# Optimization experiments

Measured on AMD Instinct MI355X. Metric: run time of the kernel, lower is better.

The kernel has to match this reference:

```python
import jax, jax.numpy as jnp
import numpy as np

D_EMBED = 1024
N_HEAD = 16
MAX_SEQ = 512
D_K = D_EMBED // N_HEAD


def setup_inputs() -> dict:
    key = jax.random.key(0)
    ks = jax.random.split(key, 10)
    B, S, D = 16, MAX_SEQ, D_EMBED
    std = 1.0 / np.sqrt(D)
    x = jax.random.normal(ks[0], (B, S, D), dtype=jnp.float32)
    Wq = jax.random.normal(ks[1], (D, D), dtype=jnp.float32) * std
    bq = jnp.zeros((D,), dtype=jnp.float32)
    Wk = jax.random.normal(ks[2], (D, D), dtype=jnp.float32) * std
    bk = jnp.zeros((D,), dtype=jnp.float32)
    Wv = jax.random.normal(ks[3], (D, D), dtype=jnp.float32) * std
    bv = jnp.zeros((D,), dtype=jnp.float32)
    Wo = jax.random.normal(ks[4], (D, D), dtype=jnp.float32) * std
    bo = jnp.zeros((D,), dtype=jnp.float32)
    rel_table = jax.random.normal(ks[5], (2 * MAX_SEQ - 1, N_HEAD), dtype=jnp.float32) * 0.02
    return {"x": x, "Wq": Wq, "bq": bq, "Wk": Wk, "bk": bk,
            "Wv": Wv, "bv": bv, "Wo": Wo, "bo": bo, "rel_table": rel_table}


def reference(x, Wq, bq, Wk, bk, Wv, bv, Wo, bo, rel_table):
    B, S, D = x.shape
    H, dk = N_HEAD, D_K
    scale = 1.0 / np.sqrt(dk)
    # QKV projections -> (B, H, S, dk)
    q = (x @ Wq.T + bq).reshape(B, S, H, dk).transpose(0, 2, 1, 3)
    k = (x @ Wk.T + bk).reshape(B, S, H, dk).transpose(0, 2, 1, 3)
    v = (x @ Wv.T + bv).reshape(B, S, H, dk).transpose(0, 2, 1, 3)
    # raw scores (B, H, S, S)
    scores = jnp.einsum('bhsd,bhtd->bhst', q * scale, k)
    # relative position bias: index[i,j] = i + (S-1-j), table (2S-1, H)
    i = jnp.arange(S)
    idx = i[:, None] + (S - 1 - i)[None, :]          # (S, S)
    bias = rel_table[idx]                             # (S, S, H)
    scores = scores + bias.transpose(2, 0, 1)[None]   # (1, H, S, S)
    probs = jax.nn.softmax(scores, axis=-1)
    attn = jnp.einsum('bhst,bhtd->bhsd', probs, v)
    attn = attn.transpose(0, 2, 1, 3).reshape(B, S, D)
    return attn @ Wo.T + bo
```

## Files before the change

kernel.cpp:

```cpp
#include <hip/hip_runtime.h>
#include <cstdint>
#include <cstddef>

typedef unsigned short u16;
typedef __attribute__((ext_vector_type(8))) short bf16x8;
typedef __attribute__((ext_vector_type(4))) float f32x4;

__device__ __forceinline__ u16 f2bf(float f) {
  unsigned u = __builtin_bit_cast(unsigned, f);
  return (u16)((u + 0x7FFFu + ((u >> 16) & 1u)) >> 16);
}

__device__ __forceinline__ void gload_lds16(const void* g, void* l) {
  __builtin_amdgcn_global_load_lds(
      (const __attribute__((address_space(1))) void*)g,
      (__attribute__((address_space(3))) void*)l,
      16, 0, 0);
}

__global__ void cast_all_kernel(const float* __restrict__ x,
                                const float* __restrict__ wq, const float* __restrict__ wk,
                                const float* __restrict__ wv, const float* __restrict__ wo,
                                u16* __restrict__ ox,
                                u16* __restrict__ oq, u16* __restrict__ ok,
                                u16* __restrict__ ov, u16* __restrict__ oo) {
  const int which = blockIdx.y;
  const float* in = which == 0 ? x  : which == 1 ? wq : which == 2 ? wk
                                    : which == 3 ? wv : wo;
  u16* out        = which == 0 ? ox : which == 1 ? oq : which == 2 ? ok
                                    : which == 3 ? ov : oo;
  const int n4 = which == 0 ? 8192 * 1024 / 4 : 262144;
  int i = blockIdx.x * blockDim.x + threadIdx.x;
  int stride = gridDim.x * blockDim.x;
  for (int idx = i; idx < n4; idx += stride) {
    float4 f = ((const float4*)in)[idx];
    ushort4 o = make_ushort4(f2bf(f.x), f2bf(f.y), f2bf(f.z), f2bf(f.w));
    ((ushort4*)out)[idx] = o;
  }
}


#define STAGE_A8(BUF, H, T)                                                    \
  { const u16* s_ = Asrc + (size_t)(H) * 131072 + (T) * 64;                    \
    u16* d_ = &lds[(BUF) * 32768 + (H) * 8192 + wid * 512];                    \
    gload_lds16(s_, d_);                                                       \
    gload_lds16(s_ + 65536, d_ + 4096); }

#define STAGE_B8(BUF, H, T)                                                    \
  { const u16* s_ = Wsrc + (size_t)(H) * 131072 + (T) * 64;                    \
    u16* d_ = &lds[(BUF) * 32768 + 16384 + (H) * 8192 + wid * 512];            \
    gload_lds16(s_, d_);                                                       \
    gload_lds16(s_ + 65536, d_ + 4096); }

#define LOAD_A8(BUF, MH)                                                       \
  _Pragma("unroll") for (int j_ = 0; j_ < 4; ++j_) {                           \
    const int r_ = ((MH) * 4 + j_) * 16 + lc;                                  \
    const int o_ = (BUF) * 32768 + abase + r_ * 64;                            \
    a[j_][0] = *(const bf16x8*)&lds[o_ + ((g ^ (r_ & 7)) * 8)];                \
    a[j_][1] = *(const bf16x8*)&lds[o_ + (((4 + g) ^ (r_ & 7)) * 8)];          \
  }

#define LOAD_B8(BUF, NH, BREG)                                                 \
  _Pragma("unroll") for (int j_ = 0; j_ < 2; ++j_) {                           \
    const int r_ = brlo + ((NH) * 2 + j_) * 16 + lc;                           \
    const int o_ = (BUF) * 32768 + bbase + r_ * 64;                            \
    BREG[j_][0] = *(const bf16x8*)&lds[o_ + ((g ^ (r_ & 7)) * 8)];             \
    BREG[j_][1] = *(const bf16x8*)&lds[o_ + (((4 + g) ^ (r_ & 7)) * 8)];       \
  }

#define MMAQ8(MH, NH, BREG)                                                    \
  __builtin_amdgcn_s_setprio(1);                                               \
  _Pragma("unroll") for (int j_ = 0; j_ < 4; ++j_)                             \
    _Pragma("unroll") for (int n_ = 0; n_ < 2; ++n_) {                         \
      acc[(MH) * 4 + j_][(NH) * 2 + n_] =                                      \
          __builtin_amdgcn_mfma_f32_16x16x32_bf16(                             \
              a[j_][0], BREG[n_][0], acc[(MH) * 4 + j_][(NH) * 2 + n_], 0, 0, 0); \
      acc[(MH) * 4 + j_][(NH) * 2 + n_] =                                      \
          __builtin_amdgcn_mfma_f32_16x16x32_bf16(                             \
              a[j_][1], BREG[n_][1], acc[(MH) * 4 + j_][(NH) * 2 + n_], 0, 0, 0); \
    }                                                                          \
  __builtin_amdgcn_s_setprio(0);

#define BAR1a                                                                  \
  __builtin_amdgcn_s_barrier();                                                \
  asm volatile("s_waitcnt lgkmcnt(0)" ::: "memory");                           \
  __builtin_amdgcn_sched_barrier(0);

#define BAR2a __builtin_amdgcn_s_barrier();

#define VMW(N) asm volatile("s_waitcnt vmcnt(" #N ")" ::: "memory");

__global__ __launch_bounds__(512, 2)
void gemm_qkv8(const u16* __restrict__ A, const u16* __restrict__ W,
               const float* __restrict__ bq, const float* __restrict__ bk,
               const float* __restrict__ bvv,
               u16* __restrict__ qout, u16* __restrict__ kout, u16* __restrict__ vt) {
  __shared__ u16 lds[65536];
  const int tid  = threadIdx.x;
  const int lane = tid & 63;
  const int wid  = tid >> 6;
  const int wr   = wid >> 2;
  const int wc   = wid & 3;
  const int lc   = lane & 15;
  const int g    = lane >> 4;

  const int orig = blockIdx.x;
  const int swz  = (orig & 7) * 48 + (orig >> 3);
  const int m0 = (swz / 12) * 256;
  const int n0 = (swz % 12) * 256;

  const int srow  = tid >> 3;
  const int scol8 = ((tid & 7) ^ (srow & 7)) * 8;
  const u16* Asrc = A + (size_t)(m0 + srow) * 1024 + scol8;
  const u16* Wsrc = W + (size_t)(n0 + srow) * 1024 + scol8;

  const int abase = wr * 8192;
  const int bbase = 16384 + (wc >> 1) * 8192;
  const int brlo  = (wc & 1) * 64;

  f32x4 acc[8][4] = {};
  bf16x8 a[4][2], bA[2][2], bB[2][2];

  STAGE_B8(0, 0, 0) STAGE_B8(0, 1, 0) STAGE_A8(0, 0, 0) STAGE_A8(0, 1, 0)
  STAGE_B8(1, 0, 1) STAGE_B8(1, 1, 1)
  VMW(4)
  __builtin_amdgcn_s_barrier();

  for (int i = 0; i < 7; ++i) {
    const int tb  = 2 * i + 1;
    const int ta2 = 2 * i + 2;
    const int tb2 = 2 * i + 3;
    LOAD_A8(0, 0) LOAD_B8(0, 0, bA) STAGE_A8(1, 0, tb) BAR1a MMAQ8(0, 0, bA) BAR2a
    LOAD_B8(0, 1, bB) STAGE_A8(1, 1, tb) BAR1a MMAQ8(0, 1, bB) BAR2a
    LOAD_A8(0, 1) STAGE_B8(0, 0, ta2) BAR1a MMAQ8(1, 0, bA) BAR2a
    STAGE_B8(0, 1, ta2) BAR1a MMAQ8(1, 1, bB) VMW(4) BAR2a
    LOAD_A8(1, 0) LOAD_B8(1, 0, bA) STAGE_A8(0, 0, ta2) BAR1a MMAQ8(0, 0, bA) BAR2a
    LOAD_B8(1, 1, bB) STAGE_A8(0, 1, ta2) BAR1a MMAQ8(0, 1, bB) BAR2a
    LOAD_A8(1, 1) STAGE_B8(1, 0, tb2) BAR1a MMAQ8(1, 0, bA) BAR2a
    STAGE_B8(1, 1, tb2) BAR1a MMAQ8(1, 1, bB) VMW(4) BAR2a
  }
  LOAD_A8(0, 0) LOAD_B8(0, 0, bA) STAGE_A8(1, 0, 15) BAR1a MMAQ8(0, 0, bA) BAR2a
  LOAD_B8(0, 1, bB) STAGE_A8(1, 1, 15) BAR1a MMAQ8(0, 1, bB) BAR2a
  LOAD_A8(0, 1) BAR1a MMAQ8(1, 0, bA) BAR2a
  BAR1a MMAQ8(1, 1, bB) VMW(0) BAR2a
  LOAD_A8(1, 0) LOAD_B8(1, 0, bA) BAR1a MMAQ8(0, 0, bA) BAR2a
  LOAD_B8(1, 1, bB) BAR1a MMAQ8(0, 1, bB) BAR2a
  LOAD_A8(1, 1) BAR1a MMAQ8(1, 0, bA) BAR2a
  BAR1a MMAQ8(1, 1, bB)

  const int region = n0 >> 10;
#pragma unroll
  for (int ni = 0; ni < 4; ++ni) {
    const int col = n0 + wc * 64 + ni * 16 + lc;
    const int nn = col & 1023;
    const float bias = region == 0 ? bq[nn] : region == 1 ? bk[nn] : bvv[nn];
#pragma unroll
    for (int mi = 0; mi < 8; ++mi) {
      const int mBase = m0 + wr * 128 + mi * 16 + g * 4;
      if (region == 0) {
#pragma unroll
        for (int r = 0; r < 4; ++r)
          qout[(size_t)(mBase + r) * 1024 + nn] = f2bf(acc[mi][ni][r] + bias);
      } else if (region == 1) {
#pragma unroll
        for (int r = 0; r < 4; ++r)
          kout[(size_t)(mBase + r) * 1024 + nn] = f2bf(acc[mi][ni][r] + bias);
      } else {
        const int batch = mBase >> 9;
        const int s = mBase & 511;
        const int h = nn >> 6;
        const int d = nn & 63;
        ushort4 ov = make_ushort4(f2bf(acc[mi][ni][0] + bias), f2bf(acc[mi][ni][1] + bias),
                                  f2bf(acc[mi][ni][2] + bias), f2bf(acc[mi][ni][3] + bias));
        *(ushort4*)&vt[((size_t)((batch * 16 + h) * 64 + d) << 9) + s] = ov;
      }
    }
  }
}

__global__ __launch_bounds__(256, 2)
void gemm_out(const u16* __restrict__ A, const u16* __restrict__ W,
              const float* __restrict__ bias, float* __restrict__ outp) {
  __shared__ u16 Alds[128 * 32];
  __shared__ u16 Blds[128 * 32];
  const int tid  = threadIdx.x;
  const int lane = tid & 63;
  const int wid  = tid >> 6;
  const int orig = blockIdx.x;
  const int swz  = (orig & 7) * 64 + (orig >> 3);
  const int m0 = (swz >> 3) * 128;
  const int n0 = (swz & 7) * 128;
  const int wm = (wid >> 1) * 64;
  const int wn = (wid & 1) * 64;

  f32x4 acc[4][4] = {};

  const int srow = tid >> 2;
  const int scol = (tid & 3) * 8;
  const u16* Ag = A + (size_t)(m0 + srow) * 1024 + scol;
  const u16* Wg = W + (size_t)(n0 + srow) * 1024 + scol;
  u16* Al = &Alds[wid * 16 * 32];
  u16* Bl = &Blds[wid * 16 * 32];

  for (int k0 = 0; k0 < 1024; k0 += 32) {
    __syncthreads();
    gload_lds16(Ag + k0,             Al);
    gload_lds16(Ag + 64 * 1024 + k0, Al + 64 * 32);
    gload_lds16(Wg + k0,             Bl);
    gload_lds16(Wg + 64 * 1024 + k0, Bl + 64 * 32);
    __syncthreads();
    bf16x8 a[4], bb[4];
#pragma unroll
    for (int i = 0; i < 4; ++i)
      a[i] = *(const bf16x8*)&Alds[(wm + i * 16 + (lane & 15)) * 32 + (lane >> 4) * 8];
#pragma unroll
    for (int i = 0; i < 4; ++i)
      bb[i] = *(const bf16x8*)&Blds[(wn + i * 16 + (lane & 15)) * 32 + (lane >> 4) * 8];
#pragma unroll
    for (int mi = 0; mi < 4; ++mi)
#pragma unroll
      for (int ni = 0; ni < 4; ++ni)
        acc[mi][ni] = __builtin_amdgcn_mfma_f32_16x16x32_bf16(a[mi], bb[ni], acc[mi][ni], 0, 0, 0);
  }

#pragma unroll
  for (int ni = 0; ni < 4; ++ni) {
    const int n = n0 + wn + ni * 16 + (lane & 15);
    const float bv = bias[n];
#pragma unroll
    for (int mi = 0; mi < 4; ++mi) {
      const int mBase = m0 + wm + mi * 16 + ((lane >> 4) << 2);
#pragma unroll
      for (int r = 0; r < 4; ++r)
        outp[(size_t)(mBase + r) * 1024 + n] = acc[mi][ni][r] + bv;
    }
  }
}

__global__ __launch_bounds__(256, 3)
void attn_kernel(const u16* __restrict__ Q, const u16* __restrict__ K,
                 const u16* __restrict__ Vt, const float* __restrict__ rel,
                 u16* __restrict__ Oa) {
  __shared__ u16 Kl[128 * 64];
  __shared__ u16 Vl[64 * 128];
  __shared__ u16 Pl[4][16 * 136];
  __shared__ float tcol[576];

  const int tid  = threadIdx.x;
  const int lane = tid & 63;
  const int wid  = tid >> 6;
  const int g    = lane >> 4;
  const int lc   = lane & 15;

  const int orig = blockIdx.x;
  const int swz  = (orig & 7) * 256 + (orig >> 3);
  const int qb    = swz & 7;
  const int bh    = swz >> 3;
  const int h     = bh & 15;
  const int batch = bh >> 4;
  const int q0    = qb * 64;

  const size_t xbase  = (size_t)batch * 512 * 1024 + (size_t)h * 64;
  const size_t vtbase = (size_t)(batch * 16 + h) * 64 * 512;

  for (int u = tid; u < 575; u += 256)
    tcol[u] = rel[(size_t)(q0 + u) * 16 + h];

#define STAGE_TILE(t)                                                              \
  {                                                                                \
    _Pragma("unroll")                                                              \
    for (int j = 0; j < 4; ++j) {                                                  \
      const int kr = j * 32 + (tid >> 3);                                          \
      const int sk = (tid & 7) ^ (kr & 7);                                         \
      gload_lds16(K + xbase + (size_t)((t) * 128 + kr) * 1024 + sk * 8,            \
                  &Kl[j * 2048 + wid * 512]);                                      \
      const int vr = j * 16 + (tid >> 4);                                          \
      const int sv = (tid & 15) ^ (vr & 7);                                        \
      gload_lds16(Vt + vtbase + (size_t)vr * 512 + (t) * 128 + sv * 8,             \
                  &Vl[j * 2048 + wid * 512]);                                      \
    }                                                                              \
  }

  STAGE_TILE(0)

  bf16x8 aq[2];
#pragma unroll
  for (int ks = 0; ks < 2; ++ks)
    aq[ks] = *(const bf16x8*)&Q[xbase + (size_t)(q0 + wid * 16 + lc) * 1024 + ks * 32 + g * 8];

  float m_run[4], l_run[4];
  f32x4 acc_o[4] = {};
#pragma unroll
  for (int r = 0; r < 4; ++r) { m_run[r] = -1e30f; l_run[r] = 0.f; }

  __syncthreads();

  const float scale = 0.125f;
  for (int t = 0; t < 4; ++t) {
    f32x4 acc[8] = {};
#pragma unroll
    for (int f = 0; f < 8; ++f) {
      const int rl = f * 16 + lc;
#pragma unroll
      for (int ks = 0; ks < 2; ++ks) {
        bf16x8 bk = *(const bf16x8*)&Kl[rl * 64 + (((ks * 4 + g) ^ (rl & 7)) * 8)];
        acc[f] = __builtin_amdgcn_mfma_f32_16x16x32_bf16(aq[ks], bk, acc[f], 0, 0, 0);
      }
    }
    const int ubase = wid * 16 + 4 * g + 511 - t * 128 - lc;
#pragma unroll
    for (int f = 0; f < 8; ++f)
#pragma unroll
      for (int r = 0; r < 4; ++r)
        acc[f][r] = acc[f][r] * scale + tcol[ubase + r - f * 16];

    float tm[4];
#pragma unroll
    for (int r = 0; r < 4; ++r) {
      float m = fmaxf(fmaxf(fmaxf(acc[0][r], acc[1][r]), fmaxf(acc[2][r], acc[3][r])),
                      fmaxf(fmaxf(acc[4][r], acc[5][r]), fmaxf(acc[6][r], acc[7][r])));
      m = fmaxf(m, __shfl_xor(m, 1));
      m = fmaxf(m, __shfl_xor(m, 2));
      m = fmaxf(m, __shfl_xor(m, 4));
      m = fmaxf(m, __shfl_xor(m, 8));
      tm[r] = m;
    }
    float al[4];
#pragma unroll
    for (int r = 0; r < 4; ++r) {
      const float mn = fmaxf(m_run[r], tm[r]);
      al[r] = __expf(m_run[r] - mn);
      m_run[r] = mn;
    }
    float ts[4] = {};
#pragma unroll
    for (int f = 0; f < 8; ++f)
#pragma unroll
      for (int r = 0; r < 4; ++r) {
        const float e = __expf(acc[f][r] - m_run[r]);
        ts[r] += e;
        Pl[wid][(4 * g + r) * 136 + f * 16 + lc] = f2bf(e);
      }
#pragma unroll
    for (int r = 0; r < 4; ++r) {
      float s = ts[r];
      s += __shfl_xor(s, 1);
      s += __shfl_xor(s, 2);
      s += __shfl_xor(s, 4);
      s += __shfl_xor(s, 8);
      l_run[r] = l_run[r] * al[r] + s;
    }
#pragma unroll
    for (int dblk = 0; dblk < 4; ++dblk)
#pragma unroll
      for (int r = 0; r < 4; ++r)
        acc_o[dblk][r] *= al[r];

#pragma unroll
    for (int ks = 0; ks < 4; ++ks) {
      bf16x8 ap = *(const bf16x8*)&Pl[wid][lc * 136 + ks * 32 + g * 8];
#pragma unroll
      for (int dblk = 0; dblk < 4; ++dblk) {
        const int dr = dblk * 16 + lc;
        bf16x8 bv = *(const bf16x8*)&Vl[dr * 128 + (((ks * 4 + g) ^ (dr & 7)) * 8)];
        acc_o[dblk] = __builtin_amdgcn_mfma_f32_16x16x32_bf16(ap, bv, acc_o[dblk], 0, 0, 0);
      }
    }

    if (t < 3) {
      __syncthreads();
      STAGE_TILE(t + 1)
      __syncthreads();
    }
  }
#undef STAGE_TILE

#pragma unroll
  for (int dblk = 0; dblk < 4; ++dblk)
#pragma unroll
    for (int r = 0; r < 4; ++r) {
      const int row = q0 + wid * 16 + 4 * g + r;
      Oa[((size_t)batch * 512 + row) * 1024 + h * 64 + dblk * 16 + lc] =
          f2bf(acc_o[dblk][r] / l_run[r]);
    }
}

extern "C" void kernel_launch(void* const* d_in, const int* in_sizes, int n_in,
                              void* d_out, int out_size, void* d_ws, size_t ws_size,
                              hipStream_t stream) {
  (void)in_sizes; (void)n_in; (void)out_size; (void)ws_size;
  const float* x   = (const float*)d_in[0];
  const float* Wq  = (const float*)d_in[1];
  const float* bq  = (const float*)d_in[2];
  const float* Wk  = (const float*)d_in[3];
  const float* bk  = (const float*)d_in[4];
  const float* Wv  = (const float*)d_in[5];
  const float* bv  = (const float*)d_in[6];
  const float* Wo  = (const float*)d_in[7];
  const float* bo  = (const float*)d_in[8];
  const float* rel = (const float*)d_in[9];
  float* out = (float*)d_out;

  u16* p = (u16*)d_ws;
  u16* xbf = p;  p += (size_t)8192 * 1024;
  u16* wqb = p;  p += (size_t)1024 * 1024;
  u16* wkb = p;  p += (size_t)1024 * 1024;
  u16* wvb = p;  p += (size_t)1024 * 1024;
  u16* wob = p;  p += (size_t)1024 * 1024;
  u16* qbf = p;  p += (size_t)8192 * 1024;
  u16* kbf = p;  p += (size_t)8192 * 1024;
  u16* vtb = p;  p += (size_t)8192 * 1024;
  u16* abf = p;  p += (size_t)8192 * 1024;

  cast_all_kernel<<<dim3(1024, 5), 256, 0, stream>>>(x, Wq, Wk, Wv, Wo,
                                                     xbf, wqb, wkb, wvb, wob);

  gemm_qkv8<<<384, 512, 0, stream>>>(xbf, wqb, bq, bk, bv, qbf, kbf, vtb);

  attn_kernel<<<2048, 256, 0, stream>>>(qbf, kbf, vtb, rel, abf);

  gemm_out<<<512, 256, 0, stream>>>(abf, wob, bo, out);
}
```

Baseline: 249.0 us.

## Process 128 query rows per attention block with lazy softmax rescaling

Each attention workgroup now handles 128 query rows (32 per wave, two MFMA row tiles), so every K/V tile staged in LDS is reused across twice as many queries and the grid is halved. The online-softmax rescale of the running max, sum and output accumulator is skipped unless some row's max grows by more than a threshold. MFMA sections are wrapped in s_setprio hints. Launch bounds drop to 2 blocks per CU to allow the higher register use, which reduces occupancy.

```diff
diff --git a/kernel.cpp b/kernel.cpp
--- a/kernel.cpp
+++ b/kernel.cpp
@@ -39,7 +39,6 @@
   }
 }
 
-
 #define STAGE_A8(BUF, H, T)                                                    \
   { const u16* s_ = Asrc + (size_t)(H) * 131072 + (T) * 64;                    \
     u16* d_ = &lds[(BUF) * 32768 + (H) * 8192 + wid * 512];                    \
@@ -237,14 +236,14 @@
   }
 }
 
-__global__ __launch_bounds__(256, 3)
+__global__ __launch_bounds__(256, 2)
 void attn_kernel(const u16* __restrict__ Q, const u16* __restrict__ K,
                  const u16* __restrict__ Vt, const float* __restrict__ rel,
                  u16* __restrict__ Oa) {
   __shared__ u16 Kl[128 * 64];
   __shared__ u16 Vl[64 * 128];
-  __shared__ u16 Pl[4][16 * 136];
-  __shared__ float tcol[576];
+  __shared__ u16 Pl[4][32 * 136];
+  __shared__ float tcol[640];
 
   const int tid  = threadIdx.x;
   const int lane = tid & 63;
@@ -253,17 +252,17 @@
   const int lc   = lane & 15;
 
   const int orig = blockIdx.x;
-  const int swz  = (orig & 7) * 256 + (orig >> 3);
-  const int qb    = swz & 7;
-  const int bh    = swz >> 3;
+  const int swz  = (orig & 7) * 128 + (orig >> 3);
+  const int qb    = swz & 3;
+  const int bh    = swz >> 2;
   const int h     = bh & 15;
   const int batch = bh >> 4;
-  const int q0    = qb * 64;
+  const int q0    = qb * 128;
 
   const size_t xbase  = (size_t)batch * 512 * 1024 + (size_t)h * 64;
   const size_t vtbase = (size_t)(batch * 16 + h) * 64 * 512;
 
-  for (int u = tid; u < 575; u += 256)
+  for (int u = tid; u < 639; u += 256)
     tcol[u] = rel[(size_t)(q0 + u) * 16 + h];
 
 #define STAGE_TILE(t)                                                              \
@@ -283,89 +282,124 @@
 
   STAGE_TILE(0)
 
-  bf16x8 aq[2];
-#pragma unroll
-  for (int ks = 0; ks < 2; ++ks)
-    aq[ks] = *(const bf16x8*)&Q[xbase + (size_t)(q0 + wid * 16 + lc) * 1024 + ks * 32 + g * 8];
-
-  float m_run[4], l_run[4];
-  f32x4 acc_o[4] = {};
-#pragma unroll
-  for (int r = 0; r < 4; ++r) { m_run[r] = -1e30f; l_run[r] = 0.f; }
+  bf16x8 aq[2][2];
+#pragma unroll
+  for (int mi = 0; mi < 2; ++mi)
+#pragma unroll
+    for (int ks = 0; ks < 2; ++ks)
+      aq[mi][ks] = *(const bf16x8*)&Q[xbase + (size_t)(q0 + wid * 32 + mi * 16 + lc) * 1024 +
+                                      ks * 32 + g * 8];
+
+  float m_run[2][4], l_run[2][4];
+  f32x4 acc_o[2][4] = {};
+#pragma unroll
+  for (int mi = 0; mi < 2; ++mi)
+#pragma unroll
+    for (int r = 0; r < 4; ++r) { m_run[mi][r] = -1e30f; l_run[mi][r] = 0.f; }
 
   __syncthreads();
 
   const float scale = 0.125f;
   for (int t = 0; t < 4; ++t) {
-    f32x4 acc[8] = {};
+    f32x4 acc[2][8] = {};
+    __builtin_amdgcn_s_setprio(1);
 #pragma unroll
     for (int f = 0; f < 8; ++f) {
       const int rl = f * 16 + lc;
 #pragma unroll
       for (int ks = 0; ks < 2; ++ks) {
         bf16x8 bk = *(const bf16x8*)&Kl[rl * 64 + (((ks * 4 + g) ^ (rl & 7)) * 8)];
-        acc[f] = __builtin_amdgcn_mfma_f32_16x16x32_bf16(aq[ks], bk, acc[f], 0, 0, 0);
-      }
-    }
-    const int ubase = wid * 16 + 4 * g + 511 - t * 128 - lc;
-#pragma unroll
-    for (int f = 0; f < 8; ++f)
+#pragma unroll
+        for (int mi = 0; mi < 2; ++mi)
+          acc[mi][f] = __builtin_amdgcn_mfma_f32_16x16x32_bf16(aq[mi][ks], bk, acc[mi][f], 0, 0, 0);
+      }
+    }
+    __builtin_amdgcn_s_setprio(0);
+
+#pragma unroll
+    for (int mi = 0; mi < 2; ++mi) {
+      const int ub = wid * 32 + mi * 16 + 4 * g + 511 - t * 128 - lc;
+#pragma unroll
+      for (int f = 0; f < 8; ++f)
+#pragma unroll
+        for (int r = 0; r < 4; ++r)
+          acc[mi][f][r] = acc[mi][f][r] * scale + tcol[ub + r - f * 16];
+    }
+
+    float tm[2][4];
+#pragma unroll
+    for (int mi = 0; mi < 2; ++mi)
+#pragma unroll
+      for (int r = 0; r < 4; ++r) {
+        float m = fmaxf(fmaxf(fmaxf(acc[mi][0][r], acc[mi][1][r]),
+                              fmaxf(acc[mi][2][r], acc[mi][3][r])),
+                        fmaxf(fmaxf(acc[mi][4][r], acc[mi][5][r]),
+                              fmaxf(acc[mi][6][r], acc[mi][7][r])));
+        m = fmaxf(m, __shfl_xor(m, 1));
+        m = fmaxf(m, __shfl_xor(m, 2));
+        m = fmaxf(m, __shfl_xor(m, 4));
+        m = fmaxf(m, __shfl_xor(m, 8));
+        tm[mi][r] = m;
+      }
+
+    bool need = false;
+#pragma unroll
+    for (int mi = 0; mi < 2; ++mi)
 #pragma unroll
       for (int r = 0; r < 4; ++r)
-        acc[f][r] = acc[f][r] * scale + tcol[ubase + r - f * 16];
-
-    float tm[4];
-#pragma unroll
-    for (int r = 0; r < 4; ++r) {
-      float m = fmaxf(fmaxf(fmaxf(acc[0][r], acc[1][r]), fmaxf(acc[2][r], acc[3][r])),
-                      fmaxf(fmaxf(acc[4][r], acc[5][r]), fmaxf(acc[6][r], acc[7][r])));
-      m = fmaxf(m, __shfl_xor(m, 1));
-      m = fmaxf(m, __shfl_xor(m, 2));
-      m = fmaxf(m, __shfl_xor(m, 4));
-      m = fmaxf(m, __shfl_xor(m, 8));
-      tm[r] = m;
-    }
-    float al[4];
-#pragma unroll
-    for (int r = 0; r < 4; ++r) {
-      const float mn = fmaxf(m_run[r], tm[r]);
-      al[r] = __expf(m_run[r] - mn);
-      m_run[r] = mn;
-    }
-    float ts[4] = {};
-#pragma unroll
-    for (int f = 0; f < 8; ++f)
+        need = need || (tm[mi][r] - m_run[mi][r] > 8.0f);
+    if (__ballot(need) != 0ull) {
+#pragma unroll
+      for (int mi = 0; mi < 2; ++mi)
+#pragma unroll
+        for (int r = 0; r < 4; ++r) {
+          const float mn = fmaxf(m_run[mi][r], tm[mi][r]);
+          const float al = __expf(m_run[mi][r] - mn);
+          m_run[mi][r] = mn;
+          l_run[mi][r] *= al;
+#pragma unroll
+          for (int dblk = 0; dblk < 4; ++dblk)
+            acc_o[mi][dblk][r] *= al;
+        }
+    }
+
+    float ts[2][4] = {};
+#pragma unroll
+    for (int mi = 0; mi < 2; ++mi)
+#pragma unroll
+      for (int f = 0; f < 8; ++f)
+#pragma unroll
+        for (int r = 0; r < 4; ++r) {
+          const float e = __expf(acc[mi][f][r] - m_run[mi][r]);
+          ts[mi][r] += e;
+          Pl[wid][(mi * 16 + 4 * g + r) * 136 + f * 16 + lc] = f2bf(e);
+        }
+#pragma unroll
+    for (int mi = 0; mi < 2; ++mi)
 #pragma unroll
       for (int r = 0; r < 4; ++r) {
-        const float e = __expf(acc[f][r] - m_run[r]);
-        ts[r] += e;
-        Pl[wid][(4 * g + r) * 136 + f * 16 + lc] = f2bf(e);
-      }
-#pragma unroll
-    for (int r = 0; r < 4; ++r) {
-      float s = ts[r];
-      s += __shfl_xor(s, 1);
-      s += __shfl_xor(s, 2);
-      s += __shfl_xor(s, 4);
-      s += __shfl_xor(s, 8);
-      l_run[r] = l_run[r] * al[r] + s;
-    }
-#pragma unroll
-    for (int dblk = 0; dblk < 4; ++dblk)
-#pragma unroll
-      for (int r = 0; r < 4; ++r)
-        acc_o[dblk][r] *= al[r];
-
+        float s = ts[mi][r];
+        s += __shfl_xor(s, 1);
+        s += __shfl_xor(s, 2);
+        s += __shfl_xor(s, 4);
+        s += __shfl_xor(s, 8);
+        l_run[mi][r] += s;
+      }
+
+    __builtin_amdgcn_s_setprio(1);
 #pragma unroll
     for (int ks = 0; ks < 4; ++ks) {
-      bf16x8 ap = *(const bf16x8*)&Pl[wid][lc * 136 + ks * 32 + g * 8];
+      bf16x8 ap0 = *(const bf16x8*)&Pl[wid][(lc) * 136 + ks * 32 + g * 8];
+      bf16x8 ap1 = *(const bf16x8*)&Pl[wid][(16 + lc) * 136 + ks * 32 + g * 8];
 #pragma unroll
       for (int dblk = 0; dblk < 4; ++dblk) {
         const int dr = dblk * 16 + lc;
         bf16x8 bv = *(const bf16x8*)&Vl[dr * 128 + (((ks * 4 + g) ^ (dr & 7)) * 8)];
-        acc_o[dblk] = __builtin_amdgcn_mfma_f32_16x16x32_bf16(ap, bv, acc_o[dblk], 0, 0, 0);
-      }
-    }
+        acc_o[0][dblk] = __builtin_amdgcn_mfma_f32_16x16x32_bf16(ap0, bv, acc_o[0][dblk], 0, 0, 0);
+        acc_o[1][dblk] = __builtin_amdgcn_mfma_f32_16x16x32_bf16(ap1, bv, acc_o[1][dblk], 0, 0, 0);
+      }
+    }
+    __builtin_amdgcn_s_setprio(0);
 
     if (t < 3) {
       __syncthreads();
@@ -376,13 +410,15 @@
 #undef STAGE_TILE
 
 #pragma unroll
-  for (int dblk = 0; dblk < 4; ++dblk)
-#pragma unroll
-    for (int r = 0; r < 4; ++r) {
-      const int row = q0 + wid * 16 + 4 * g + r;
-      Oa[((size_t)batch * 512 + row) * 1024 + h * 64 + dblk * 16 + lc] =
-          f2bf(acc_o[dblk][r] / l_run[r]);
-    }
+  for (int mi = 0; mi < 2; ++mi)
+#pragma unroll
+    for (int dblk = 0; dblk < 4; ++dblk)
+#pragma unroll
+      for (int r = 0; r < 4; ++r) {
+        const int row = q0 + wid * 32 + mi * 16 + 4 * g + r;
+        Oa[((size_t)batch * 512 + row) * 1024 + h * 64 + dblk * 16 + lc] =
+            f2bf(acc_o[mi][dblk][r] / l_run[mi][r]);
+      }
 }
 
 extern "C" void kernel_launch(void* const* d_in, const int* in_sizes, int n_in,
@@ -417,7 +453,7 @@
 
   gemm_qkv8<<<384, 512, 0, stream>>>(xbf, wqb, bq, bk, bv, qbf, kbf, vtb);
 
-  attn_kernel<<<2048, 256, 0, stream>>>(qbf, kbf, vtb, rel, abf);
+  attn_kernel<<<1024, 256, 0, stream>>>(qbf, kbf, vtb, rel, abf);
 
   gemm_out<<<512, 256, 0, stream>>>(abf, wob, bo, out);
 }
```

Result: no change. 247.2 us (-0.7%).
